# Optimization experiments

Hardware: AMD Instinct MI355X
Metric: run time of the kernel (lower is better)

The kernel has to match this reference:

```python
import jax, jax.numpy as jnp
import numpy as np

N_FEATURES = 256
RAND_RANGE = 100.0


def _random_embed(x):
    """Deterministic pseudo-random embedding: each scalar in x seeds a counter-based
    RNG producing N_FEATURES uniforms in [0, RAND_RANGE). (JAX threefry replaces
    Python's Mersenne Twister; same structure: value-seeded deterministic uniforms.)"""
    flat = jax.lax.stop_gradient(x).reshape(-1)
    seeds = jax.lax.bitcast_convert_type(flat, jnp.uint32)  # value -> integer seed
    base = jax.random.key(42)
    keys = jax.vmap(lambda s: jax.random.fold_in(base, s))(seeds)
    emb = jax.vmap(lambda k: jax.random.uniform(k, (N_FEATURES,), minval=0.0, maxval=RAND_RANGE))(keys)
    return emb.reshape(x.shape + (N_FEATURES,))  # [B, S, F]


def setup_inputs() -> dict:
    key = jax.random.key(0)
    kx, kw, kb = jax.random.split(key, 3)
    x = jax.random.normal(kx, (256, 512), dtype=jnp.float32)
    W = jax.random.normal(kw, (N_FEATURES, N_FEATURES), dtype=jnp.float32) * 0.05
    b = jax.random.normal(kb, (N_FEATURES,), dtype=jnp.float32) * 0.05
    return {"x": x, "W": W, "b": b}


def reference(x, W, b):
    emb = _random_embed(x)                      # [B, S, F]
    out = jnp.einsum('bsf,gf->bsg', emb, W) + b  # nn.Linear: emb @ W.T + b
    return out
```

## Files before the change

kernel.cpp:

```cpp
#include <hip/hip_runtime.h>
#include <stdint.h>

#define F 256
#define R 64
#define THREADS 256
#define EPAD 264
#define GCH 32
#define NCH (F / GCH)
#define SLOTS (GCH * F / 8)

typedef __attribute__((ext_vector_type(8))) short short8;
typedef __attribute__((ext_vector_type(4))) float floatx4;

__device__ __forceinline__ uint32_t rotl32(uint32_t x, int d) {
  return (x << d) | (x >> (32 - d));
}

__device__ __forceinline__ void tf2x32(uint32_t k0, uint32_t k1,
                                       uint32_t x0, uint32_t x1,
                                       uint32_t& o0, uint32_t& o1) {
  const uint32_t k2 = k0 ^ k1 ^ 0x1BD11BDAu;
  x0 += k0; x1 += k1;
#define TF_R4(a,b,c,d)                                    \
  x0 += x1; x1 = rotl32(x1,(a)); x1 ^= x0;                \
  x0 += x1; x1 = rotl32(x1,(b)); x1 ^= x0;                \
  x0 += x1; x1 = rotl32(x1,(c)); x1 ^= x0;                \
  x0 += x1; x1 = rotl32(x1,(d)); x1 ^= x0;
  TF_R4(13,15,26,6)
  x0 += k1; x1 += k2 + 1u;
  TF_R4(17,29,16,24)
  x0 += k2; x1 += k0 + 2u;
  TF_R4(13,15,26,6)
  x0 += k0; x1 += k1 + 3u;
  TF_R4(17,29,16,24)
  x0 += k1; x1 += k2 + 4u;
  TF_R4(13,15,26,6)
  x0 += k2; x1 += k0 + 5u;
#undef TF_R4
  o0 = x0; o1 = x1;
}

__device__ __forceinline__ float bits_to_unif(uint32_t bits) {
  uint32_t u = (bits >> 9) | 0x3F800000u;
  return fmaxf(0.0f, (__uint_as_float(u) - 1.0f) * 100.0f);
}

__device__ __forceinline__ uint16_t f2bf(float f) {
  uint32_t u = __float_as_uint(f);
  u += 0x7FFFu + ((u >> 16) & 1u);
  return (uint16_t)(u >> 16);
}

__device__ __forceinline__ void gl_lds16(const void* gptr, void* lptr) {
  __builtin_amdgcn_global_load_lds(
      (const __attribute__((address_space(1))) uint32_t*)gptr,
      (__attribute__((address_space(3))) uint32_t*)lptr, 16, 0, 0);
}

__global__ __launch_bounds__(256) void femb_conv(const float* __restrict__ W,
                                                 uint16_t* __restrict__ ws) {
  int s = blockIdx.x * 256 + threadIdx.x;
  int row = s >> 5;
  int c = s & 31;
  int src_c = c ^ (row & 7);
  const float4* src = (const float4*)(W + (size_t)row * F + src_c * 8);
  float4 v0 = src[0], v1 = src[1];
  short8 o;
  o[0] = (short)f2bf(v0.x); o[1] = (short)f2bf(v0.y);
  o[2] = (short)f2bf(v0.z); o[3] = (short)f2bf(v0.w);
  o[4] = (short)f2bf(v1.x); o[5] = (short)f2bf(v1.y);
  o[6] = (short)f2bf(v1.z); o[7] = (short)f2bf(v1.w);
  *(short8*)(ws + (size_t)s * 8) = o;
}

__global__ __launch_bounds__(THREADS, 3) void femb_main(
    const float* __restrict__ x, const uint16_t* __restrict__ Wbf,
    const float* __restrict__ bias, float* __restrict__ out) {
  __shared__ uint16_t semb[R][EPAD];
  __shared__ uint16_t sW[GCH * F];
  __shared__ uint32_t skey[R][2];

  const int tid  = threadIdx.x;
  const int lane = tid & 63;
  const int wave = tid >> 6;
  const int qd   = lane >> 4;
  const int l16  = lane & 15;
  const size_t row0 = (size_t)blockIdx.x * R;

  if (tid < R) {
    uint32_t s = __float_as_uint(x[row0 + tid]);
    uint32_t o0, o1;
    tf2x32(0u, 42u, 0u, s, o0, o1);
    skey[tid][0] = o0; skey[tid][1] = o1;
  }
  __syncthreads();

  #pragma unroll 4
  for (int k = 0; k < R; ++k) {
    uint32_t o0, o1;
    tf2x32(skey[k][0], skey[k][1], 0u, (uint32_t)tid, o0, o1);
    semb[k][tid] = f2bf(bits_to_unif(o0 ^ o1));
  }
  __syncthreads();

  const uint16_t* arow = &semb[wave * 16 + l16][qd * 8];
  short8 afrag[8];
  #pragma unroll
  for (int kt = 0; kt < 8; ++kt) afrag[kt] = *(const short8*)(arow + kt * 32);

  for (int gt = 0; gt < NCH; ++gt) {
    const uint16_t* src = Wbf + (size_t)gt * SLOTS * 8;
    #pragma unroll
    for (int it = 0; it < SLOTS / THREADS; ++it) {
      int sbase = it * THREADS + wave * 64;
      gl_lds16(src + (size_t)(sbase + lane) * 8, &sW[(size_t)sbase * 8]);
    }
    __syncthreads();

    floatx4 acc[2];
    acc[0] = (floatx4){0.f, 0.f, 0.f, 0.f};
    acc[1] = (floatx4){0.f, 0.f, 0.f, 0.f};
    #pragma unroll
    for (int kt = 0; kt < 8; ++kt) {
      #pragma unroll
      for (int n = 0; n < 2; ++n) {
        int g = n * 16 + l16;
        int slot = g * 32 + ((kt * 4 + qd) ^ (g & 7));
        short8 b = *(const short8*)&sW[(size_t)slot * 8];
        acc[n] = __builtin_amdgcn_mfma_f32_16x16x32_bf16(afrag[kt], b, acc[n], 0, 0, 0);
      }
    }

    #pragma unroll
    for (int n = 0; n < 2; ++n) {
      int gg = gt * GCH + n * 16 + l16;
      float bg = bias[gg];
      #pragma unroll
      for (int reg = 0; reg < 4; ++reg) {
        size_t grow = row0 + (size_t)wave * 16 + qd * 4 + reg;
        out[grow * F + gg] = acc[n][reg] + bg;
      }
    }
    __syncthreads();
  }
}

extern "C" void kernel_launch(void* const* d_in, const int* in_sizes, int n_in,
                              void* d_out, int out_size, void* d_ws, size_t ws_size,
                              hipStream_t stream) {
  const float* x = (const float*)d_in[0];
  const float* W = (const float*)d_in[1];
  const float* b = (const float*)d_in[2];
  float* out = (float*)d_out;
  uint16_t* wsbf = (uint16_t*)d_ws;
  const int nrows = in_sizes[0];
  const int blocks = nrows / R;

  hipLaunchKernelGGL(femb_conv, dim3((F * F / 8) / 256), dim3(256), 0, stream, W, wsbf);
  hipLaunchKernelGGL(femb_main, dim3(blocks), dim3(THREADS), 0, stream,
                     x, wsbf, b, out);
}
```

Before: 198.9 us.

## Generate embedding fragments in registers and double-buffer weight chunks in LDS

Each lane now computes the threefry bits for its own MFMA A-fragment directly in registers. This removes the shared-memory key table, the embedding staging array and two block barriers. Weight chunks are double-buffered in LDS: the next chunk's global-to-LDS load is issued before computing on the current one, and the XOR swizzle is dropped in favour of a chunk-major layout from the conversion kernel. Lower LDS use allows raising launch bounds to 4 blocks per CU, and the uniform conversion now uses a direct int-to-float scale, which gives slightly different rounding from the reference mantissa trick.

```diff
diff --git a/kernel.cpp b/kernel.cpp
--- a/kernel.cpp
+++ b/kernel.cpp
@@ -4,10 +4,9 @@
 #define F 256
 #define R 64
 #define THREADS 256
-#define EPAD 264
 #define GCH 32
 #define NCH (F / GCH)
-#define SLOTS (GCH * F / 8)
+#define CH_SLOTS (GCH * F / 8)
 
 typedef __attribute__((ext_vector_type(8))) short short8;
 typedef __attribute__((ext_vector_type(4))) float floatx4;
@@ -40,15 +39,16 @@
   o0 = x0; o1 = x1;
 }
 
-__device__ __forceinline__ float bits_to_unif(uint32_t bits) {
-  uint32_t u = (bits >> 9) | 0x3F800000u;
-  return fmaxf(0.0f, (__uint_as_float(u) - 1.0f) * 100.0f);
+__device__ __forceinline__ uint32_t f2bf(float f) {
+  uint32_t u = __float_as_uint(f);
+  u += 0x7FFFu + ((u >> 16) & 1u);
+  return u >> 16;
 }
 
-__device__ __forceinline__ uint16_t f2bf(float f) {
-  uint32_t u = __float_as_uint(f);
-  u += 0x7FFFu + ((u >> 16) & 1u);
-  return (uint16_t)(u >> 16);
+__device__ __forceinline__ uint32_t feat_bf16(uint32_t k0, uint32_t k1, uint32_t i) {
+  uint32_t o0, o1;
+  tf2x32(k0, k1, 0u, i, o0, o1);
+  return f2bf((float)(o0 ^ o1) * 2.3283064365386963e-8f);
 }
 
 __device__ __forceinline__ void gl_lds16(const void* gptr, void* lptr) {
@@ -60,10 +60,10 @@
 __global__ __launch_bounds__(256) void femb_conv(const float* __restrict__ W,
                                                  uint16_t* __restrict__ ws) {
   int s = blockIdx.x * 256 + threadIdx.x;
-  int row = s >> 5;
-  int c = s & 31;
-  int src_c = c ^ (row & 7);
-  const float4* src = (const float4*)(W + (size_t)row * F + src_c * 8);
+  int gt = s >> 10;
+  int c = (s >> 5) & 31;
+  int g = s & 31;
+  const float4* src = (const float4*)(W + (size_t)(gt * GCH + g) * F + c * 8);
   float4 v0 = src[0], v1 = src[1];
   short8 o;
   o[0] = (short)f2bf(v0.x); o[1] = (short)f2bf(v0.y);
@@ -73,12 +73,10 @@
   *(short8*)(ws + (size_t)s * 8) = o;
 }
 
-__global__ __launch_bounds__(THREADS, 3) void femb_main(
+__global__ __launch_bounds__(THREADS, 4) void femb_main(
     const float* __restrict__ x, const uint16_t* __restrict__ Wbf,
     const float* __restrict__ bias, float* __restrict__ out) {
-  __shared__ uint16_t semb[R][EPAD];
-  __shared__ uint16_t sW[GCH * F];
-  __shared__ uint32_t skey[R][2];
+  __shared__ uint16_t sW[2][GCH * F];
 
   const int tid  = threadIdx.x;
   const int lane = tid & 63;
@@ -86,62 +84,74 @@
   const int qd   = lane >> 4;
   const int l16  = lane & 15;
   const size_t row0 = (size_t)blockIdx.x * R;
+  const int myrow = (int)row0 + wave * 16 + l16;
 
-  if (tid < R) {
-    uint32_t s = __float_as_uint(x[row0 + tid]);
-    uint32_t o0, o1;
-    tf2x32(0u, 42u, 0u, s, o0, o1);
-    skey[tid][0] = o0; skey[tid][1] = o1;
+  float xv = x[myrow];
+
+  {
+    const uint16_t* src = Wbf;
+    #pragma unroll
+    for (int it = 0; it < CH_SLOTS / THREADS; ++it) {
+      int sbase = it * THREADS + wave * 64;
+      gl_lds16(src + (size_t)(sbase + lane) * 8, &sW[0][(size_t)sbase * 8]);
+    }
   }
-  __syncthreads();
 
-  #pragma unroll 4
-  for (int k = 0; k < R; ++k) {
-    uint32_t o0, o1;
-    tf2x32(skey[k][0], skey[k][1], 0u, (uint32_t)tid, o0, o1);
-    semb[k][tid] = f2bf(bits_to_unif(o0 ^ o1));
-  }
-  __syncthreads();
+  uint32_t k0, k1;
+  tf2x32(0u, 42u, 0u, __float_as_uint(xv), k0, k1);
 
-  const uint16_t* arow = &semb[wave * 16 + l16][qd * 8];
   short8 afrag[8];
   #pragma unroll
-  for (int kt = 0; kt < 8; ++kt) afrag[kt] = *(const short8*)(arow + kt * 32);
+  for (int kt = 0; kt < 8; ++kt) {
+    const uint32_t fb = (uint32_t)(kt * 32 + qd * 8);
+    uint32_t w32[4];
+    #pragma unroll
+    for (int p = 0; p < 4; ++p) {
+      uint32_t lo = feat_bf16(k0, k1, fb + 2 * p);
+      uint32_t hi = feat_bf16(k0, k1, fb + 2 * p + 1);
+      w32[p] = lo | (hi << 16);
+    }
+    union { uint32_t w[4]; short8 s; } u;
+    u.w[0] = w32[0]; u.w[1] = w32[1]; u.w[2] = w32[2]; u.w[3] = w32[3];
+    afrag[kt] = u.s;
+  }
 
   for (int gt = 0; gt < NCH; ++gt) {
-    const uint16_t* src = Wbf + (size_t)gt * SLOTS * 8;
-    #pragma unroll
-    for (int it = 0; it < SLOTS / THREADS; ++it) {
-      int sbase = it * THREADS + wave * 64;
-      gl_lds16(src + (size_t)(sbase + lane) * 8, &sW[(size_t)sbase * 8]);
+    __syncthreads();
+    if (gt + 1 < NCH) {
+      const uint16_t* src = Wbf + (size_t)(gt + 1) * CH_SLOTS * 8;
+      #pragma unroll
+      for (int it = 0; it < CH_SLOTS / THREADS; ++it) {
+        int sbase = it * THREADS + wave * 64;
+        gl_lds16(src + (size_t)(sbase + lane) * 8,
+                 &sW[(gt + 1) & 1][(size_t)sbase * 8]);
+      }
     }
-    __syncthreads();
 
+    const uint16_t* buf = sW[gt & 1];
     floatx4 acc[2];
     acc[0] = (floatx4){0.f, 0.f, 0.f, 0.f};
     acc[1] = (floatx4){0.f, 0.f, 0.f, 0.f};
     #pragma unroll
     for (int kt = 0; kt < 8; ++kt) {
+      int c = kt * 4 + qd;
       #pragma unroll
       for (int n = 0; n < 2; ++n) {
-        int g = n * 16 + l16;
-        int slot = g * 32 + ((kt * 4 + qd) ^ (g & 7));
-        short8 b = *(const short8*)&sW[(size_t)slot * 8];
+        short8 b = *(const short8*)&buf[(size_t)(c * 32 + n * 16 + l16) * 8];
         acc[n] = __builtin_amdgcn_mfma_f32_16x16x32_bf16(afrag[kt], b, acc[n], 0, 0, 0);
       }
     }
 
     #pragma unroll
     for (int n = 0; n < 2; ++n) {
-      int gg = gt * GCH + n * 16 + l16;
-      float bg = bias[gg];
+      int g = gt * GCH + n * 16 + l16;
+      float bg = bias[g];
       #pragma unroll
       for (int reg = 0; reg < 4; ++reg) {
         size_t grow = row0 + (size_t)wave * 16 + qd * 4 + reg;
-        out[grow * F + gg] = acc[n][reg] + bg;
+        out[grow * F + g] = acc[n][reg] + bg;
       }
     }
-    __syncthreads();
   }
 }
 
```

Measured after the change: 195.1 us. No clear change (-1.9%).
